# Optimization experiments

Measured on AMD Instinct MI355X. Metric: run time of the kernel, lower is better.

## Reference

```python
import jax, jax.numpy as jnp
import numpy as np

CS = 64          # chunk_size
CP = CS - 1      # causal_padding
H = 8            # heads
DH = 64          # dim_head
SCALE = DH ** -0.5


def rotate_half(x):
    x1, x2 = jnp.split(x, 2, axis=-1)
    return jnp.concatenate((-x2, x1), axis=-1)


def apply_rope(t, freqs):
    rd = freqs.shape[-1]
    t_rot, t_pass = t[..., :rd], t[..., rd:]
    t_rot = t_rot * jnp.cos(freqs) + rotate_half(t_rot) * jnp.sin(freqs)
    return jnp.concatenate((t_rot, t_pass), axis=-1)


def setup_inputs() -> dict:
    key = jax.random.key(0)
    ks = jax.random.split(key, 10)
    b, n, dim = 4, 4096, 1024
    k_chunks, r, rlen = 64, 2, 128
    inner = H * DH
    return {
        "x": jax.random.normal(ks[0], (b, n, dim), dtype=jnp.float32),
        "context": jax.random.normal(ks[1], (b, k_chunks, r, rlen, dim), dtype=jnp.float32),
        "q_pos_emb": jax.random.normal(ks[2], (1, 1, CS, DH), dtype=jnp.float32),
        "k_pos_emb": jax.random.normal(ks[3], (1, 1, rlen, DH), dtype=jnp.float32),
        "Wq": jax.random.normal(ks[4], (dim, inner), dtype=jnp.float32) * 0.02,
        "Wk": jax.random.normal(ks[5], (dim, inner), dtype=jnp.float32) * 0.02,
        "Wv": jax.random.normal(ks[6], (dim, inner), dtype=jnp.float32) * 0.02,
        "Wo": jax.random.normal(ks[7], (inner, dim), dtype=jnp.float32) * 0.02,
        "bo": jnp.zeros((dim,), dtype=jnp.float32),
        "null_k": jax.random.normal(ks[8], (inner,), dtype=jnp.float32),
        "null_v": jax.random.normal(ks[9], (inner,), dtype=jnp.float32),
    }


def reference(x, context, q_pos_emb, k_pos_emb, Wq, Wk, Wv, Wo, bo, null_k, null_v):
    b, n, dim = x.shape
    _, k_chunks, r, rlen, _ = context.shape
    # causal shift: drop first CP tokens, pad CP zeros at end (F.pad with -CP)
    xs = jnp.pad(x[:, CP:], ((0, 0), (0, CP), (0, 0)))
    seq_index = (n // CS) * CS
    rem = n - seq_index
    xs = xs[:, :seq_index]                                   # [b, k*CS, dim]
    # shift q rope the same way; pad region gets freqs=0 -> identity rotation
    qpe = jnp.pad(q_pos_emb[:, :, CP:], ((0, 0), (0, 0), (0, CP), (0, 0)))
    kpe = jnp.tile(k_pos_emb, (1, 1, r, 1))                  # [1,1,r*rlen,DH]
    bk = b * k_chunks
    xc = xs.reshape(bk, CS, dim)
    ctx = context.reshape(bk, r * rlen, dim)
    # projections -> [bk, h, seq, dh]
    q = (xc @ Wq).reshape(bk, CS, H, DH).transpose(0, 2, 1, 3) * SCALE
    k = (ctx @ Wk).reshape(bk, r * rlen, H, DH).transpose(0, 2, 1, 3)
    v = (ctx @ Wv).reshape(bk, r * rlen, H, DH).transpose(0, 2, 1, 3)
    q = apply_rope(q, qpe)
    k = apply_rope(k, kpe)
    # null kv prepend
    nk = jnp.broadcast_to(null_k.reshape(1, H, 1, DH), (bk, H, 1, DH))
    nv = jnp.broadcast_to(null_v.reshape(1, H, 1, DH), (bk, H, 1, DH))
    k = jnp.concatenate((nk, k), axis=2)
    v = jnp.concatenate((nv, v), axis=2)
    sim = jnp.einsum('bhid,bhjd->bhij', q, k)
    attn = jax.nn.softmax(sim, axis=-1)
    o = jnp.einsum('bhij,bhjd->bhid', attn, v)
    o = o.transpose(0, 2, 1, 3).reshape(bk, CS, H * DH)
    o = o @ Wo + bo                                          # [bk, CS, dim]
    o = o.reshape(b, k_chunks * CS, dim)
    # unshift: pad CP zeros at front, trim CP - rem from end
    o = jnp.concatenate(
        (jnp.zeros((b, CP, dim), o.dtype), o[:, :k_chunks * CS - CP + rem]), axis=1)
    return o
```

## Files before the change

### kernel.cpp

```cpp
#include <hip/hip_runtime.h>


#define DEV __device__ __forceinline__

typedef __bf16 bf16x8 __attribute__((ext_vector_type(8)));
typedef float f32x4 __attribute__((ext_vector_type(4)));

DEV unsigned short f2bf(float f) {
  union { float f; unsigned int u; } v; v.f = f;
  unsigned int u = v.u;
  unsigned int r = (u + 0x7FFFu + ((u >> 16) & 1u)) >> 16;
  return (unsigned short)r;
}
DEV float bf2f(unsigned short h) {
  union { unsigned int u; float f; } v; v.u = ((unsigned int)h) << 16;
  return v.f;
}
DEV float bfelem(bf16x8 v, int i) {
  union { bf16x8 v; unsigned short u[8]; } t; t.v = v;
  return bf2f(t.u[i]);
}
DEV unsigned int pkbf(unsigned int hi, unsigned int lo) {
  return __builtin_amdgcn_perm(hi, lo, 0x07060302u);
}
DEV unsigned int pk2(float lo, float hi) {
  return ((unsigned int)f2bf(hi) << 16) | f2bf(lo);
}

DEV void ldst16(const void* g, void* l) {
  __builtin_amdgcn_global_load_lds(
      (const __attribute__((address_space(1))) void*)g,
      (__attribute__((address_space(3))) void*)l, 16, 0, 0);
}

DEV void bar() { __builtin_amdgcn_s_barrier(); }
#define VMCNT4 asm volatile("s_waitcnt vmcnt(4)" ::: "memory")
#define VMCNT0 asm volatile("s_waitcnt vmcnt(0)" ::: "memory")

__global__ __launch_bounds__(256) void prep_k(const float* __restrict__ Wq,
                                              const float* __restrict__ Wk,
                                              const float* __restrict__ Wv,
                                              const float* __restrict__ Wo,
                                              const float* __restrict__ qpe,
                                              const float* __restrict__ kpe,
                                              unsigned short* __restrict__ Wqt,
                                              unsigned short* __restrict__ Wkt,
                                              unsigned short* __restrict__ Wvt,
                                              unsigned short* __restrict__ Wot,
                                              float* __restrict__ ck, float* __restrict__ sk,
                                              float* __restrict__ cq, float* __restrict__ sq,
                                              float* __restrict__ out) {
  __shared__ float tl[64][65];
  int blk = blockIdx.x;
  int tid = threadIdx.x;
  if (blk < 512) {
    int mat = blk >> 7, loc = blk & 127;
    const float* W;
    unsigned short* Wt;
    int R, C;
    float scale = 1.0f;
    if (mat == 0)      { W = Wq; Wt = Wqt; R = 1024; C = 512; scale = 0.125f; }
    else if (mat == 1) { W = Wk; Wt = Wkt; R = 1024; C = 512; }
    else if (mat == 2) { W = Wv; Wt = Wvt; R = 1024; C = 512; }
    else               { W = Wo; Wt = Wot; R = 512;  C = 1024; }
    int nct = C >> 6;
    int rt = loc / nct, ct = loc % nct;
    int r0 = rt << 6, c0 = ct << 6;
    #pragma unroll
    for (int i = 0; i < 16; ++i) {
      int flat = i * 256 + tid;
      int rr = flat >> 6, cc = flat & 63;
      tl[rr][cc] = W[(size_t)(r0 + rr) * C + c0 + cc] * scale;
    }
    __syncthreads();
    #pragma unroll
    for (int i = 0; i < 16; ++i) {
      int flat = i * 256 + tid;
      int cc = flat >> 6, rr = flat & 63;
      Wt[(size_t)(c0 + cc) * R + r0 + rr] = f2bf(tl[rr][cc]);
    }
  } else if (blk < 764) {
    int r = blk - 512;
    int b = r / 63, rr = r % 63;
    float4 z = {0.f, 0.f, 0.f, 0.f};
    *(float4*)(out + (((size_t)(b * 4096 + rr)) << 10) + tid * 4) = z;
  } else {
    int t = (blk - 764) * 256 + tid;
    float f = kpe[t];
    ck[t] = cosf(f);
    sk[t] = sinf(f);
    if (t < 64) {
      float g = qpe[63 * 64 + t];
      cq[t] = cosf(g);
      sq[t] = sinf(g);
    }
  }
}

__global__ __launch_bounds__(256) void cast_all(const float* __restrict__ ctx,
                                                const float* __restrict__ x,
                                                unsigned short* __restrict__ ctxb,
                                                unsigned short* __restrict__ xb) {
  int id = blockIdx.x;
  if (id < 32768) {
    size_t base = ((size_t)id * 256 + threadIdx.x) * 8;
    uint4 lo = *(const uint4*)(ctx + base);
    uint4 hi = *(const uint4*)(ctx + base + 4);
    uint4 pk;
    pk.x = pkbf(lo.y, lo.x);
    pk.y = pkbf(lo.w, lo.z);
    pk.z = pkbf(hi.y, hi.x);
    pk.w = pkbf(hi.w, hi.z);
    *(uint4*)(ctxb + base) = pk;
  } else {
    size_t e = ((size_t)(id - 32768) * 256 + threadIdx.x) * 8;
    int m = (int)(e >> 10), c = (int)(e & 1023);
    int b = m >> 12, t = m & 4095;
    uint4 pk = {0, 0, 0, 0};
    if (t <= 4032) {
      const float* s = x + (((size_t)(b << 12) + t + 63) << 10) + c;
      uint4 lo = *(const uint4*)s;
      uint4 hi = *(const uint4*)(s + 4);
      pk.x = pkbf(lo.y, lo.x);
      pk.y = pkbf(lo.w, lo.z);
      pk.z = pkbf(hi.y, hi.x);
      pk.w = pkbf(hi.w, hi.z);
    }
    *(uint4*)(xb + e) = pk;
  }
}

DEV bf16x8 rdfrag(const unsigned short* b, int row, int c) {
  return *(const bf16x8*)((const char*)b + row * 128 + ((c ^ (row & 7)) << 4));
}
DEV bf16x8 rdfrag512(const unsigned short* b, int row, int c) {
  return *(const bf16x8*)((const char*)b + row * 512 + ((c ^ (row & 7)) << 4));
}

DEV void rdA(const unsigned short* bufA, int wm, int ln15, int l4, int mtb,
             bf16x8 (&af)[2][2]) {
  #pragma unroll
  for (int mq = 0; mq < 2; ++mq)
    #pragma unroll
    for (int kk = 0; kk < 2; ++kk)
      af[mq][kk] = rdfrag(bufA, wm + (mtb + mq) * 16 + ln15, kk * 4 + l4);
}

DEV void rdB(const unsigned short* bufB, int wn, int ln15, int l4, bf16x8 (&bf)[4][2]) {
  #pragma unroll
  for (int nt = 0; nt < 4; ++nt)
    #pragma unroll
    for (int kk = 0; kk < 2; ++kk)
      bf[nt][kk] = rdfrag(bufB, wn + nt * 16 + ln15, kk * 4 + l4);
}

template <int MTB>
DEV void mfma16(const bf16x8 (&af)[2][2], const bf16x8 (&bf)[4][2], f32x4 (&acc)[8][4]) {
  __builtin_amdgcn_s_setprio(1);
  #pragma unroll
  for (int mq = 0; mq < 2; ++mq)
    #pragma unroll
    for (int nt = 0; nt < 4; ++nt)
      #pragma unroll
      for (int kk = 0; kk < 2; ++kk)
        acc[MTB + mq][nt] = __builtin_amdgcn_mfma_f32_16x16x32_bf16(
            af[mq][kk], bf[nt][kk], acc[MTB + mq][nt], 0, 0, 0);
  __builtin_amdgcn_s_setprio(0);
}

DEV void stg(unsigned short* buf, const unsigned short* src, int r0, int w,
             int Lrow, int srcC, int k0, int h, int ldK) {
  #pragma unroll
  for (int qq = 0; qq < 2; ++qq) {
    int q = 2 * h + qq;
    ldst16(src + (size_t)(r0 + q * 64 + w * 8 + Lrow) * ldK + (k0 + srcC * 8),
           (char*)buf + ((q * 512 + w * 64) << 4));
  }
}

template <int KD>
DEV void kloop8(const unsigned short* __restrict__ A, const unsigned short* __restrict__ B,
                unsigned short* sh, f32x4 (&acc)[8][4], int m0, int n0, int tid) {
  unsigned short* A0b = sh;
  unsigned short* A1b = sh + 16384;
  unsigned short* B0b = sh + 32768;
  unsigned short* B1b = sh + 49152;
  int w = tid >> 6, lane = tid & 63;
  int wm = (w & 1) * 128, wn = (w >> 1) * 64;
  int ln15 = lane & 15, l4 = lane >> 4;
  int Lrow = lane >> 3;
  int srcC = (lane & 7) ^ (Lrow & 7);
  const int MSK = KD - 1;

  stg(A0b, A, m0, w, Lrow, srcC, 0, 0, KD);
  stg(A0b, A, m0, w, Lrow, srcC, 0, 1, KD);
  stg(B0b, B, n0, w, Lrow, srcC, 0, 0, KD);
  stg(B0b, B, n0, w, Lrow, srcC, 0, 1, KD);
  stg(B1b, B, n0, w, Lrow, srcC, 64, 0, KD);
  stg(B1b, B, n0, w, Lrow, srcC, 64, 1, KD);
  VMCNT4;
  bar();

  for (int it = 0; it < KD / 128; ++it) {
    const int k0 = it * 128;
    bf16x8 af[2][2], bf[4][2];

    rdB(B0b, wn, ln15, l4, bf);
    rdA(A0b, wm, ln15, l4, 0, af);
    stg(A1b, A, m0, w, Lrow, srcC, k0 + 64, 0, KD);
    bar(); mfma16<0>(af, bf, acc); bar();

    rdA(A0b, wm, ln15, l4, 2, af);
    stg(A1b, A, m0, w, Lrow, srcC, k0 + 64, 1, KD);
    bar(); mfma16<2>(af, bf, acc); bar();

    rdA(A0b, wm, ln15, l4, 4, af);
    stg(B0b, B, n0, w, Lrow, srcC, (k0 + 128) & MSK, 0, KD);
    bar(); mfma16<4>(af, bf, acc); bar();

    rdA(A0b, wm, ln15, l4, 6, af);
    stg(B0b, B, n0, w, Lrow, srcC, (k0 + 128) & MSK, 1, KD);
    VMCNT4;
    bar(); mfma16<6>(af, bf, acc); bar();

    rdB(B1b, wn, ln15, l4, bf);
    rdA(A1b, wm, ln15, l4, 0, af);
    stg(A0b, A, m0, w, Lrow, srcC, (k0 + 128) & MSK, 0, KD);
    bar(); mfma16<0>(af, bf, acc); bar();

    rdA(A1b, wm, ln15, l4, 2, af);
    stg(A0b, A, m0, w, Lrow, srcC, (k0 + 128) & MSK, 1, KD);
    bar(); mfma16<2>(af, bf, acc); bar();

    rdA(A1b, wm, ln15, l4, 4, af);
    stg(B1b, B, n0, w, Lrow, srcC, (k0 + 192) & MSK, 0, KD);
    bar(); mfma16<4>(af, bf, acc); bar();

    rdA(A1b, wm, ln15, l4, 6, af);
    stg(B1b, B, n0, w, Lrow, srcC, (k0 + 192) & MSK, 1, KD);
    VMCNT4;
    bar(); mfma16<6>(af, bf, acc); bar();
  }

  VMCNT0;
  bar();
}

__global__ __launch_bounds__(512, 2) void proj8(const unsigned short* __restrict__ ctxb,
                                                const unsigned short* __restrict__ xb,
                                                const unsigned short* __restrict__ Wkt,
                                                const unsigned short* __restrict__ Wvt,
                                                const unsigned short* __restrict__ Wqt,
                                                unsigned short* __restrict__ kb,
                                                unsigned short* __restrict__ vtg,
                                                unsigned short* __restrict__ qbuf,
                                                const float* __restrict__ ck,
                                                const float* __restrict__ sk,
                                                const float* __restrict__ cq,
                                                const float* __restrict__ sq) {
  __shared__ unsigned short sh[65536];
  int id = blockIdx.x;
  int mode, m0, n0;
  const unsigned short *A, *B;
  if (id < 1024) {
    int x = (id & 7) + 8 * (id >> 5);
    int j = (id >> 3) & 3;
    int y = j & 1, z = j >> 1;
    mode = z;
    A = ctxb; B = z ? Wvt : Wkt;
    m0 = x << 8; n0 = y << 8;
  } else {
    int t = id - 1024;
    int x = (t & 7) + 8 * (t >> 4);
    int y = (t >> 3) & 1;
    mode = 2;
    A = xb; B = Wqt;
    m0 = x << 8; n0 = y << 8;
  }
  int tid = threadIdx.x, w = tid >> 6, lane = tid & 63;
  int wm = (w & 1) * 128, wn = (w >> 1) * 64;
  int ln15 = lane & 15, l4 = lane >> 4;

  f32x4 acc[8][4] = {};
  kloop8<1024>(A, B, sh, acc, m0, n0, tid);

  if (mode == 0) {
    #pragma unroll
    for (int mt = 0; mt < 8; ++mt)
      #pragma unroll
      for (int r = 0; r < 4; ++r) {
        int m = m0 + wm + mt * 16 + l4 * 4 + r;
        int fib = (m & 127) << 6;
        #pragma unroll
        for (int nt = 0; nt < 4; ++nt) {
          int d = nt * 16 + ln15;
          float partner = acc[mt][nt ^ 2][r];
          float val = acc[mt][nt][r] * ck[fib + d] + (nt < 2 ? -partner : partner) * sk[fib + d];
          kb[(size_t)m * 512 + n0 + wn + d] = f2bf(val);
        }
      }
  } else if (mode == 1) {
    #pragma unroll
    for (int mt = 0; mt < 8; ++mt)
      #pragma unroll
      for (int nt = 0; nt < 4; ++nt)
        #pragma unroll
        for (int r = 0; r < 4; ++r) {
          int ml = wm + mt * 16 + l4 * 4 + r;
          int nl = wn + nt * 16 + ln15;
          int mc = ml >> 3, me = ml & 7;
          *(unsigned short*)((char*)sh + nl * 512 + ((mc ^ (nl & 31)) << 4) + me * 2) =
              f2bf(acc[mt][nt][r]);
        }
    __syncthreads();
    #pragma unroll
    for (int i = 0; i < 16; ++i) {
      int flat = i * 512 + tid;
      int nl = flat >> 5, mc = flat & 31;
      uint4 v = *(const uint4*)((const char*)sh + nl * 512 + ((mc ^ (nl & 31)) << 4));
      *(uint4*)(vtg + (size_t)(n0 + nl) * 65536 + m0 + mc * 8) = v;
    }
  } else {
    #pragma unroll
    for (int mt = 0; mt < 8; ++mt)
      #pragma unroll
      for (int nt = 0; nt < 4; ++nt)
        #pragma unroll
        for (int r = 0; r < 4; ++r) {
          int m = m0 + wm + mt * 16 + l4 * 4 + r;
          int n = n0 + wn + nt * 16 + ln15;
          float val = acc[mt][nt][r];
          if ((m & 63) == 0) {
            int d = nt * 16 + ln15;
            float partner = acc[mt][nt ^ 2][r];
            val = val * cq[d] + (nt < 2 ? -partner : partner) * sq[d];
          }
          qbuf[(size_t)m * 512 + n] = f2bf(val);
        }
  }
}

__global__ __launch_bounds__(512, 2) void out8(const unsigned short* __restrict__ A,
                                               const unsigned short* __restrict__ B,
                                               const float* __restrict__ bias,
                                               float* __restrict__ out) {
  __shared__ unsigned short sh[65536];
  int id = blockIdx.x;
  int x = (id & 7) + 8 * (id >> 5);
  int y = (id >> 3) & 3;
  int m0 = x << 8, n0 = y << 8;
  int tid = threadIdx.x, w = tid >> 6, lane = tid & 63;
  int wm = (w & 1) * 128, wn = (w >> 1) * 64;
  int ln15 = lane & 15, l4 = lane >> 4;

  f32x4 acc[8][4] = {};
  kloop8<512>(A, B, sh, acc, m0, n0, tid);

  #pragma unroll
  for (int mt = 0; mt < 8; ++mt)
    #pragma unroll
    for (int nt = 0; nt < 4; ++nt)
      #pragma unroll
      for (int r = 0; r < 4; ++r) {
        int m = m0 + wm + mt * 16 + l4 * 4 + r;
        int n = n0 + wn + nt * 16 + ln15;
        int b = m >> 12, t = m & 4095;
        if (t <= 4032)
          out[((size_t)((b << 12) + t + 63)) * 1024 + n] = acc[mt][nt][r] + bias[n];
      }
}

__global__ __launch_bounds__(256) void attn_kernel(const unsigned short* __restrict__ qb,
                                                   const unsigned short* __restrict__ kb,
                                                   const unsigned short* __restrict__ vtg,
                                                   const float* __restrict__ nullk,
                                                   const float* __restrict__ nullv,
                                                   unsigned short* __restrict__ ob) {
  __shared__ unsigned short qs[64 * 64];
  __shared__ unsigned short ks[256 * 64];
  __shared__ unsigned short vs[64 * 256];
  int id = blockIdx.x;
  int bc = (id & 7) + 8 * (id >> 6);
  int h = (id >> 3) & 7;
  int tid = threadIdx.x, w = tid >> 6, lane = tid & 63;
  int ln15 = lane & 15, l4 = lane >> 4;
  int Lrow = lane >> 3, srcC = (lane & 7) ^ (Lrow & 7);

  #pragma unroll
  for (int q8 = 0; q8 < 2; ++q8) {
    int t = w * 2 + q8;
    ldst16(qb + (size_t)(bc * 64 + t * 8 + Lrow) * 512 + h * 64 + srcC * 8, (char*)qs + t * 1024);
  }
  #pragma unroll
  for (int q8 = 0; q8 < 8; ++q8) {
    int t = w * 8 + q8;
    ldst16(kb + (size_t)(bc * 256 + t * 8 + Lrow) * 512 + h * 64 + srcC * 8, (char*)ks + t * 1024);
  }
  #pragma unroll
  for (int q8 = 0; q8 < 8; ++q8) {
    int t = w * 8 + q8;
    int dd = t * 2 + (lane >> 5);
    int cl = (lane & 31) ^ (dd & 7);
    ldst16(vtg + (size_t)(h * 64 + dd) * 65536 + bc * 256 + cl * 8, (char*)vs + t * 1024);
  }
  __syncthreads();

  int q = w * 16 + ln15;

  float ns = 0.f;
  {
    bf16x8 q0 = rdfrag(qs, q, l4 * 2);
    bf16x8 q1 = rdfrag(qs, q, l4 * 2 + 1);
    const float* nkp = nullk + h * 64 + l4 * 16;
    #pragma unroll
    for (int i = 0; i < 8; ++i) ns += bfelem(q0, i) * nkp[i];
    #pragma unroll
    for (int i = 0; i < 8; ++i) ns += bfelem(q1, i) * nkp[8 + i];
    ns += __shfl_xor(ns, 16);
    ns += __shfl_xor(ns, 32);
  }
  float rnull = __expf(ns);

  f32x4 acc[16] = {};
  #pragma unroll
  for (int k32 = 0; k32 < 2; ++k32) {
    int c = k32 * 4 + l4;
    bf16x8 bq = rdfrag(qs, q, c);
    #pragma unroll
    for (int nt = 0; nt < 16; ++nt) {
      bf16x8 ak = rdfrag(ks, nt * 16 + ln15, c);
      acc[nt] = __builtin_amdgcn_mfma_f32_16x16x32_bf16(ak, bq, acc[nt], 0, 0, 0);
    }
  }

  float s = 0.f;
  #pragma unroll
  for (int nt = 0; nt < 16; ++nt)
    #pragma unroll
    for (int r = 0; r < 4; ++r) {
      float p = __expf(acc[nt][r]);
      acc[nt][r] = p;
      s += p;
    }
  s += __shfl_xor(s, 16);
  s += __shfl_xor(s, 32);
  float rsum = s + rnull;

  __syncthreads();

  #pragma unroll
  for (int nt = 0; nt < 16; ++nt) {
    unsigned int w0 = pk2(acc[nt][0], acc[nt][1]);
    unsigned int w1 = pk2(acc[nt][2], acc[nt][3]);
    int j = nt * 16 + l4 * 4;
    int cj = j >> 3;
    int off = (j & 7) * 2;
    uint2 v = {w0, w1};
    *(uint2*)((char*)ks + q * 512 + ((cj ^ (q & 7)) << 4) + off) = v;
  }
  f32x4 oacc[4] = {};
  #pragma unroll
  for (int kk = 0; kk < 8; ++kk) {
    int c = kk * 4 + l4;
    bf16x8 bp = rdfrag512(ks, q, c);
    #pragma unroll
    for (int nt = 0; nt < 4; ++nt) {
      bf16x8 av = rdfrag512(vs, nt * 16 + ln15, c);
      oacc[nt] = __builtin_amdgcn_mfma_f32_16x16x32_bf16(av, bp, oacc[nt], 0, 0, 0);
    }
  }

  float inv = 1.0f / rsum;
  #pragma unroll
  for (int nt = 0; nt < 4; ++nt) {
    const float* nvp = nullv + h * 64 + nt * 16 + l4 * 4;
    float4 nv4 = *(const float4*)nvp;
    float o0 = (oacc[nt][0] + rnull * nv4.x) * inv;
    float o1 = (oacc[nt][1] + rnull * nv4.y) * inv;
    float o2 = (oacc[nt][2] + rnull * nv4.z) * inv;
    float o3 = (oacc[nt][3] + rnull * nv4.w) * inv;
    uint2 v = {pk2(o0, o1), pk2(o2, o3)};
    *(uint2*)(ob + ((size_t)(bc * 64 + q) * 8 + h) * 64 + nt * 16 + l4 * 4) = v;
  }
}

extern "C" void kernel_launch(void* const* d_in, const int* in_sizes, int n_in,
                              void* d_out, int out_size, void* d_ws, size_t ws_size,
                              hipStream_t stream) {
  const float* x = (const float*)d_in[0];
  const float* ctx = (const float*)d_in[1];
  const float* qpe = (const float*)d_in[2];
  const float* kpe = (const float*)d_in[3];
  const float* Wq = (const float*)d_in[4];
  const float* Wk = (const float*)d_in[5];
  const float* Wv = (const float*)d_in[6];
  const float* Wo = (const float*)d_in[7];
  const float* bo = (const float*)d_in[8];
  const float* nk = (const float*)d_in[9];
  const float* nv = (const float*)d_in[10];
  float* out = (float*)d_out;
  char* ws = (char*)d_ws;

  unsigned short* Wqt  = (unsigned short*)(ws + 0);
  unsigned short* Wkt  = (unsigned short*)(ws + 1048576);
  unsigned short* Wvt  = (unsigned short*)(ws + 2097152);
  unsigned short* Wot  = (unsigned short*)(ws + 3145728);
  float* cosk = (float*)(ws + 4194304);
  float* sink = (float*)(ws + 4227072);
  float* cosq = (float*)(ws + 4259840);
  float* sinq = (float*)(ws + 4260096);
  unsigned short* qb   = (unsigned short*)(ws + 8388608);
  unsigned short* kb   = (unsigned short*)(ws + 25165824);
  unsigned short* vtg  = (unsigned short*)(ws + 92274688);
  unsigned short* obuf = (unsigned short*)(ws + 159383552);
  unsigned short* xb   = (unsigned short*)(ws + 176160768);
  unsigned short* ctxb = (unsigned short*)(ws + 209715200);

  prep_k<<<796, 256, 0, stream>>>(Wq, Wk, Wv, Wo, qpe, kpe, Wqt, Wkt, Wvt, Wot,
                                  cosk, sink, cosq, sinq, out);

  cast_all<<<40960, 256, 0, stream>>>(ctx, x, ctxb, xb);

  proj8<<<1152, 512, 0, stream>>>(ctxb, xb, Wkt, Wvt, Wqt, kb, vtg, qb,
                                  cosk, sink, cosq, sinq);

  attn_kernel<<<2048, 256, 0, stream>>>(qb, kb, vtg, nk, nv, obuf);

  out8<<<256, 512, 0, stream>>>(obuf, Wot, bo, out);
}
```

Measured before the change: 673.8 us.

## Triple-buffer A tiles and double-buffer B in GEMM k-loop

Replaces the two-stage A/B shared-memory ping-pong in the projection and output GEMM main loops with a new loop that advances one 64-wide k-step per iteration. A now rotates through three LDS buffers and B through two. Each global stage issues a full tile (four loads) at once, and A is prefetched two steps ahead to give loads more time to land before they are consumed. Shared memory per block grows from 128 KiB to 160 KiB, which fills the CU's LDS with a single block and leaves no room for any other workgroup.

```diff
diff --git a/kernel.cpp b/kernel.cpp
--- a/kernel.cpp
+++ b/kernel.cpp
@@ -168,76 +168,55 @@
   __builtin_amdgcn_s_setprio(0);
 }
 
-DEV void stg(unsigned short* buf, const unsigned short* src, int r0, int w,
-             int Lrow, int srcC, int k0, int h, int ldK) {
-  #pragma unroll
-  for (int qq = 0; qq < 2; ++qq) {
-    int q = 2 * h + qq;
+DEV void stgF(unsigned short* buf, const unsigned short* src, int r0, int w,
+              int Lrow, int srcC, int k0, int ldK) {
+  #pragma unroll
+  for (int q = 0; q < 4; ++q) {
     ldst16(src + (size_t)(r0 + q * 64 + w * 8 + Lrow) * ldK + (k0 + srcC * 8),
            (char*)buf + ((q * 512 + w * 64) << 4));
   }
 }
 
 template <int KD>
-DEV void kloop8(const unsigned short* __restrict__ A, const unsigned short* __restrict__ B,
+DEV void kloopP(const unsigned short* __restrict__ A, const unsigned short* __restrict__ B,
                 unsigned short* sh, f32x4 (&acc)[8][4], int m0, int n0, int tid) {
-  unsigned short* A0b = sh;
-  unsigned short* A1b = sh + 16384;
-  unsigned short* B0b = sh + 32768;
-  unsigned short* B1b = sh + 49152;
+  unsigned short* Abase = sh;
+  unsigned short* Bbase = sh + 49152;
   int w = tid >> 6, lane = tid & 63;
   int wm = (w & 1) * 128, wn = (w >> 1) * 64;
   int ln15 = lane & 15, l4 = lane >> 4;
   int Lrow = lane >> 3;
   int srcC = (lane & 7) ^ (Lrow & 7);
   const int MSK = KD - 1;
-
-  stg(A0b, A, m0, w, Lrow, srcC, 0, 0, KD);
-  stg(A0b, A, m0, w, Lrow, srcC, 0, 1, KD);
-  stg(B0b, B, n0, w, Lrow, srcC, 0, 0, KD);
-  stg(B0b, B, n0, w, Lrow, srcC, 0, 1, KD);
-  stg(B1b, B, n0, w, Lrow, srcC, 64, 0, KD);
-  stg(B1b, B, n0, w, Lrow, srcC, 64, 1, KD);
+  const int NT = KD / 64;
+
+  stgF(Abase,         A, m0, w, Lrow, srcC, 0, KD);
+  stgF(Bbase,         B, n0, w, Lrow, srcC, 0, KD);
+  stgF(Abase + 16384, A, m0, w, Lrow, srcC, 64, KD);
   VMCNT4;
   bar();
 
-  for (int it = 0; it < KD / 128; ++it) {
-    const int k0 = it * 128;
+  for (int t = 0; t < NT; ++t) {
+    const int k0 = t * 64;
+    unsigned short* Ar = Abase + (t % 3) * 16384;
+    unsigned short* As = Abase + ((t + 2) % 3) * 16384;
+    unsigned short* Br = Bbase + (t & 1) * 16384;
+    unsigned short* Bs = Bbase + ((t + 1) & 1) * 16384;
     bf16x8 af[2][2], bf[4][2];
 
-    rdB(B0b, wn, ln15, l4, bf);
-    rdA(A0b, wm, ln15, l4, 0, af);
-    stg(A1b, A, m0, w, Lrow, srcC, k0 + 64, 0, KD);
+    rdB(Br, wn, ln15, l4, bf);
+    rdA(Ar, wm, ln15, l4, 0, af);
+    stgF(Bs, B, n0, w, Lrow, srcC, (k0 + 64) & MSK, KD);
     bar(); mfma16<0>(af, bf, acc); bar();
 
-    rdA(A0b, wm, ln15, l4, 2, af);
-    stg(A1b, A, m0, w, Lrow, srcC, k0 + 64, 1, KD);
+    rdA(Ar, wm, ln15, l4, 2, af);
     bar(); mfma16<2>(af, bf, acc); bar();
 
-    rdA(A0b, wm, ln15, l4, 4, af);
-    stg(B0b, B, n0, w, Lrow, srcC, (k0 + 128) & MSK, 0, KD);
+    rdA(Ar, wm, ln15, l4, 4, af);
+    stgF(As, A, m0, w, Lrow, srcC, (k0 + 128) & MSK, KD);
     bar(); mfma16<4>(af, bf, acc); bar();
 
-    rdA(A0b, wm, ln15, l4, 6, af);
-    stg(B0b, B, n0, w, Lrow, srcC, (k0 + 128) & MSK, 1, KD);
-    VMCNT4;
-    bar(); mfma16<6>(af, bf, acc); bar();
-
-    rdB(B1b, wn, ln15, l4, bf);
-    rdA(A1b, wm, ln15, l4, 0, af);
-    stg(A0b, A, m0, w, Lrow, srcC, (k0 + 128) & MSK, 0, KD);
-    bar(); mfma16<0>(af, bf, acc); bar();
-
-    rdA(A1b, wm, ln15, l4, 2, af);
-    stg(A0b, A, m0, w, Lrow, srcC, (k0 + 128) & MSK, 1, KD);
-    bar(); mfma16<2>(af, bf, acc); bar();
-
-    rdA(A1b, wm, ln15, l4, 4, af);
-    stg(B1b, B, n0, w, Lrow, srcC, (k0 + 192) & MSK, 0, KD);
-    bar(); mfma16<4>(af, bf, acc); bar();
-
-    rdA(A1b, wm, ln15, l4, 6, af);
-    stg(B1b, B, n0, w, Lrow, srcC, (k0 + 192) & MSK, 1, KD);
+    rdA(Ar, wm, ln15, l4, 6, af);
     VMCNT4;
     bar(); mfma16<6>(af, bf, acc); bar();
   }
@@ -258,7 +237,7 @@
                                                 const float* __restrict__ sk,
                                                 const float* __restrict__ cq,
                                                 const float* __restrict__ sq) {
-  __shared__ unsigned short sh[65536];
+  __shared__ unsigned short sh[81920];
   int id = blockIdx.x;
   int mode, m0, n0;
   const unsigned short *A, *B;
@@ -282,7 +261,7 @@
   int ln15 = lane & 15, l4 = lane >> 4;
 
   f32x4 acc[8][4] = {};
-  kloop8<1024>(A, B, sh, acc, m0, n0, tid);
+  kloopP<1024>(A, B, sh, acc, m0, n0, tid);
 
   if (mode == 0) {
     #pragma unroll
@@ -344,7 +323,7 @@
                                                const unsigned short* __restrict__ B,
                                                const float* __restrict__ bias,
                                                float* __restrict__ out) {
-  __shared__ unsigned short sh[65536];
+  __shared__ unsigned short sh[81920];
   int id = blockIdx.x;
   int x = (id & 7) + 8 * (id >> 5);
   int y = (id >> 3) & 3;
@@ -354,7 +333,7 @@
   int ln15 = lane & 15, l4 = lane >> 4;
 
   f32x4 acc[8][4] = {};
-  kloop8<512>(A, B, sh, acc, m0, n0, tid);
+  kloopP<512>(A, B, sh, acc, m0, n0, tid);
 
   #pragma unroll
   for (int mt = 0; mt < 8; ++mt)
```

Result: slower. 688.9 us (+2.2%).
